# Performance work log

Hardware: AMD Instinct MI355X
Metric: run time of the kernel (lower is better)

Reference implementation:

```python
import jax, jax.numpy as jnp
import numpy as np


def bilinear_sample(img, xs, ys):
    # img: [C,H,W]; xs, ys: [Ho,Wo] fractional source coords (pixel units).
    # Zero-fill outside the image, matching grid_sample(padding_mode='zeros').
    C, H, W = img.shape
    x0f = jnp.floor(xs); y0f = jnp.floor(ys)
    wx = xs - x0f; wy = ys - y0f
    x0 = x0f.astype(jnp.int32); y0 = y0f.astype(jnp.int32)

    def gather(yi, xi):
        inb = ((xi >= 0) & (xi <= W - 1) & (yi >= 0) & (yi <= H - 1))
        xc = jnp.clip(xi, 0, W - 1); yc = jnp.clip(yi, 0, H - 1)
        return img[:, yc, xc] * inb[None].astype(img.dtype)

    v00 = gather(y0,     x0)
    v01 = gather(y0,     x0 + 1)
    v10 = gather(y0 + 1, x0)
    v11 = gather(y0 + 1, x0 + 1)
    return (v00 * (1 - wx) * (1 - wy) + v01 * wx * (1 - wy)
            + v10 * (1 - wx) * wy + v11 * wx * wy)


def setup_inputs() -> dict:
    key = jax.random.key(0)
    k1, k2 = jax.random.split(key)
    frame = jax.random.uniform(k1, (1, 4, 1080, 1920), dtype=jnp.float32)
    # last channel is the alpha/transparency mask: fully opaque frame
    frame = frame.at[:, -1].set(1.0)
    canvas = jax.random.uniform(k2, (1, 4, 2048, 3072), dtype=jnp.float32)
    # realistic near-identity homography: small rotation + translation + tiny perspective
    th = 0.02
    Hmat = jnp.array([[np.cos(th), -np.sin(th), 400.0],
                      [np.sin(th),  np.cos(th), 300.0],
                      [1e-6,        0.0,        1.0]], dtype=jnp.float32)
    return {"frame": frame, "Hmat": Hmat, "canvas": canvas}


def reference(frame, Hmat, canvas):
    # Homography warp of `frame` into the canvas coordinate grid (inverse warp +
    # bilinear resample), then 'over' alpha-compositing onto the canvas
    # (merge_frame), fused into one pass over the canvas buffer.
    _, C, Hc, Wc = canvas.shape
    Hinv = jnp.linalg.inv(Hmat)
    dt = frame.dtype
    ys, xs = jnp.meshgrid(jnp.arange(Hc, dtype=dt), jnp.arange(Wc, dtype=dt), indexing='ij')
    coords = jnp.stack([xs, ys, jnp.ones_like(xs)])          # [3,Hc,Wc]
    src = jnp.einsum('ij,jhw->ihw', Hinv, coords)            # [3,Hc,Wc]
    sx = src[0] / src[2]
    sy = src[1] / src[2]
    warped = bilinear_sample(frame[0], sx, sy)               # [C,Hc,Wc]
    a_s = warped[-1:]                                        # source alpha
    a_c = canvas[0, -1:]                                     # canvas alpha
    out_rgb = warped[:-1] * a_s + canvas[0, :-1] * a_c * (1.0 - a_s)
    out_a = a_s + a_c * (1.0 - a_s)
    return jnp.concatenate([out_rgb, out_a], axis=0)[None]   # [1,C,Hc,Wc]
```

## Files before the change

kernel.cpp:

```cpp
#include <hip/hip_runtime.h>


#define FH 1080
#define FW 1920
#define CH 2048
#define CW 3072
#define FHW (FH * FW)
#define CHW (CH * CW)

__global__ __launch_bounds__(256) void pano_kernel(
    const float* __restrict__ frame,
    const float* __restrict__ Hm,
    const float* __restrict__ canvas,
    float* __restrict__ out)
{
    const int x = blockIdx.x * 256 + threadIdx.x;
    const int y = blockIdx.y;
    const int pix = y * CW + x;

    const float a  = Hm[0], b  = Hm[1], c  = Hm[2];
    const float d  = Hm[3], e  = Hm[4], f  = Hm[5];
    const float g  = Hm[6], hh = Hm[7], i9 = Hm[8];

    const float A0 = e * i9 - f * hh, A1 = c * hh - b * i9, A2 = b * f - c * e;
    const float B0 = f * g  - d * i9, B1 = a * i9 - c * g,  B2 = c * d - a * f;
    const float C0 = d * hh - e * g,  C1 = b * g  - a * hh, C2 = a * e - b * d;

    const float xf = (float)x, yf = (float)y;
    const float u = A0 * xf + A1 * yf + A2;
    const float v = B0 * xf + B1 * yf + B2;
    const float w = C0 * xf + C1 * yf + C2;
    const float sx = u / w;
    const float sy = v / w;

    const float x0f = floorf(sx);
    const float y0f = floorf(sy);
    const float wx = sx - x0f;
    const float wy = sy - y0f;
    const int x0 = (int)x0f;
    const int y0 = (int)y0f;

    const float c0 = canvas[0 * CHW + pix];
    const float c1 = canvas[1 * CHW + pix];
    const float c2 = canvas[2 * CHW + pix];
    const float ac = canvas[3 * CHW + pix];

    float w0 = 0.f, w1 = 0.f, w2 = 0.f, as = 0.f;

    if (x0 >= -1 && x0 <= FW - 1 && y0 >= -1 && y0 <= FH - 1) {
        const int x1 = x0 + 1, y1 = y0 + 1;
        const float mx0 = (x0 >= 0 && x0 <= FW - 1) ? 1.f : 0.f;
        const float mx1 = (x1 >= 0 && x1 <= FW - 1) ? 1.f : 0.f;
        const float my0 = (y0 >= 0 && y0 <= FH - 1) ? 1.f : 0.f;
        const float my1 = (y1 >= 0 && y1 <= FH - 1) ? 1.f : 0.f;
        const int xc0 = min(max(x0, 0), FW - 1);
        const int xc1 = min(max(x1, 0), FW - 1);
        const int yc0 = min(max(y0, 0), FH - 1);
        const int yc1 = min(max(y1, 0), FH - 1);

        const float w00 = (1.f - wx) * (1.f - wy) * mx0 * my0;
        const float w01 = wx * (1.f - wy) * mx1 * my0;
        const float w10 = (1.f - wx) * wy * mx0 * my1;
        const float w11 = wx * wy * mx1 * my1;

        const int i00 = yc0 * FW + xc0;
        const int i01 = yc0 * FW + xc1;
        const int i10 = yc1 * FW + xc0;
        const int i11 = yc1 * FW + xc1;

        #pragma unroll
        for (int ch = 0; ch < 4; ++ch) {
            const float* fp = frame + ch * FHW;
            const float val = w00 * fp[i00] + w01 * fp[i01]
                            + w10 * fp[i10] + w11 * fp[i11];
            if (ch == 0) w0 = val;
            else if (ch == 1) w1 = val;
            else if (ch == 2) w2 = val;
            else as = val;
        }
    }

    const float k = ac * (1.f - as);
    out[0 * CHW + pix] = w0 * as + c0 * k;
    out[1 * CHW + pix] = w1 * as + c1 * k;
    out[2 * CHW + pix] = w2 * as + c2 * k;
    out[3 * CHW + pix] = as + k;
}

extern "C" void kernel_launch(void* const* d_in, const int* in_sizes, int n_in,
                              void* d_out, int out_size, void* d_ws, size_t ws_size,
                              hipStream_t stream) {
    const float* frame  = (const float*)d_in[0];
    const float* Hm     = (const float*)d_in[1];
    const float* canvas = (const float*)d_in[2];
    float* out = (float*)d_out;

    dim3 block(256, 1, 1);
    dim3 grid(CW / 256, CH, 1);
    pano_kernel<<<grid, block, 0, stream>>>(frame, Hm, canvas, out);
}
```

Baseline: 203.7 us.

## Process four pixels per thread with vector canvas I/O and nontemporal stores

Each thread now handles four consecutive canvas pixels. It loads the canvas with 128-bit vector loads and writes the output with nontemporal vector stores. The homography numerators are advanced incrementally, the division is replaced by a fast reciprocal, and a fully-interior fast path skips the clamping and masking. This aims to cut memory instruction count and per-pixel ALU overhead in a bandwidth-bound kernel. In exchange, each thread issues a serial chain of gathers, and the approximate reciprocal may differ slightly from the exact division.

After: 213.6 us. 1.05x slower.

```diff
diff --git a/kernel.cpp b/kernel.cpp
--- a/kernel.cpp
+++ b/kernel.cpp
@@ -8,15 +8,17 @@
 #define FHW (FH * FW)
 #define CHW (CH * CW)
 
+typedef float f32x4 __attribute__((ext_vector_type(4)));
+
 __global__ __launch_bounds__(256) void pano_kernel(
     const float* __restrict__ frame,
     const float* __restrict__ Hm,
     const float* __restrict__ canvas,
     float* __restrict__ out)
 {
-    const int x = blockIdx.x * 256 + threadIdx.x;
-    const int y = blockIdx.y;
-    const int pix = y * CW + x;
+    const int x4  = blockIdx.x * 1024 + threadIdx.x * 4;
+    const int y   = blockIdx.y;
+    const int pix = y * CW + x4;
 
     const float a  = Hm[0], b  = Hm[1], c  = Hm[2];
     const float d  = Hm[3], e  = Hm[4], f  = Hm[5];
@@ -26,65 +28,95 @@
     const float B0 = f * g  - d * i9, B1 = a * i9 - c * g,  B2 = c * d - a * f;
     const float C0 = d * hh - e * g,  C1 = b * g  - a * hh, C2 = a * e - b * d;
 
-    const float xf = (float)x, yf = (float)y;
-    const float u = A0 * xf + A1 * yf + A2;
-    const float v = B0 * xf + B1 * yf + B2;
-    const float w = C0 * xf + C1 * yf + C2;
-    const float sx = u / w;
-    const float sy = v / w;
+    const f32x4 cv0 = *(const f32x4*)(canvas + 0 * CHW + pix);
+    const f32x4 cv1 = *(const f32x4*)(canvas + 1 * CHW + pix);
+    const f32x4 cv2 = *(const f32x4*)(canvas + 2 * CHW + pix);
+    const f32x4 cva = *(const f32x4*)(canvas + 3 * CHW + pix);
 
-    const float x0f = floorf(sx);
-    const float y0f = floorf(sy);
-    const float wx = sx - x0f;
-    const float wy = sy - y0f;
-    const int x0 = (int)x0f;
-    const int y0 = (int)y0f;
+    const float xf = (float)x4, yf = (float)y;
+    float u = A0 * xf + A1 * yf + A2;
+    float v = B0 * xf + B1 * yf + B2;
+    float w = C0 * xf + C1 * yf + C2;
 
-    const float c0 = canvas[0 * CHW + pix];
-    const float c1 = canvas[1 * CHW + pix];
-    const float c2 = canvas[2 * CHW + pix];
-    const float ac = canvas[3 * CHW + pix];
+    f32x4 o0, o1, o2, oa;
 
-    float w0 = 0.f, w1 = 0.f, w2 = 0.f, as = 0.f;
+    #pragma unroll
+    for (int j = 0; j < 4; ++j) {
+        const float rw = __builtin_amdgcn_rcpf(w);
+        const float sx = u * rw;
+        const float sy = v * rw;
 
-    if (x0 >= -1 && x0 <= FW - 1 && y0 >= -1 && y0 <= FH - 1) {
-        const int x1 = x0 + 1, y1 = y0 + 1;
-        const float mx0 = (x0 >= 0 && x0 <= FW - 1) ? 1.f : 0.f;
-        const float mx1 = (x1 >= 0 && x1 <= FW - 1) ? 1.f : 0.f;
-        const float my0 = (y0 >= 0 && y0 <= FH - 1) ? 1.f : 0.f;
-        const float my1 = (y1 >= 0 && y1 <= FH - 1) ? 1.f : 0.f;
-        const int xc0 = min(max(x0, 0), FW - 1);
-        const int xc1 = min(max(x1, 0), FW - 1);
-        const int yc0 = min(max(y0, 0), FH - 1);
-        const int yc1 = min(max(y1, 0), FH - 1);
+        const float x0f = floorf(sx);
+        const float y0f = floorf(sy);
+        const float wx = sx - x0f;
+        const float wy = sy - y0f;
+        const int x0 = (int)x0f;
+        const int y0 = (int)y0f;
 
-        const float w00 = (1.f - wx) * (1.f - wy) * mx0 * my0;
-        const float w01 = wx * (1.f - wy) * mx1 * my0;
-        const float w10 = (1.f - wx) * wy * mx0 * my1;
-        const float w11 = wx * wy * mx1 * my1;
+        float w0 = 0.f, w1 = 0.f, w2 = 0.f, as = 0.f;
 
-        const int i00 = yc0 * FW + xc0;
-        const int i01 = yc0 * FW + xc1;
-        const int i10 = yc1 * FW + xc0;
-        const int i11 = yc1 * FW + xc1;
+        if (x0 >= 0 && x0 <= FW - 2 && y0 >= 0 && y0 <= FH - 2) {
+            const float w00 = (1.f - wx) * (1.f - wy);
+            const float w01 = wx * (1.f - wy);
+            const float w10 = (1.f - wx) * wy;
+            const float w11 = wx * wy;
+            const int i00 = y0 * FW + x0;
+            #pragma unroll
+            for (int ch = 0; ch < 4; ++ch) {
+                const float* fp = frame + ch * FHW;
+                const float val = w00 * fp[i00]      + w01 * fp[i00 + 1]
+                                + w10 * fp[i00 + FW] + w11 * fp[i00 + FW + 1];
+                if      (ch == 0) w0 = val;
+                else if (ch == 1) w1 = val;
+                else if (ch == 2) w2 = val;
+                else              as = val;
+            }
+        } else if (x0 >= -1 && x0 <= FW - 1 && y0 >= -1 && y0 <= FH - 1) {
+            const int x1 = x0 + 1, y1 = y0 + 1;
+            const float mx0 = (x0 >= 0) ? 1.f : 0.f;
+            const float mx1 = (x1 <= FW - 1) ? 1.f : 0.f;
+            const float my0 = (y0 >= 0) ? 1.f : 0.f;
+            const float my1 = (y1 <= FH - 1) ? 1.f : 0.f;
+            const int xc0 = min(max(x0, 0), FW - 1);
+            const int xc1 = min(max(x1, 0), FW - 1);
+            const int yc0 = min(max(y0, 0), FH - 1);
+            const int yc1 = min(max(y1, 0), FH - 1);
 
-        #pragma unroll
-        for (int ch = 0; ch < 4; ++ch) {
-            const float* fp = frame + ch * FHW;
-            const float val = w00 * fp[i00] + w01 * fp[i01]
-                            + w10 * fp[i10] + w11 * fp[i11];
-            if (ch == 0) w0 = val;
-            else if (ch == 1) w1 = val;
-            else if (ch == 2) w2 = val;
-            else as = val;
+            const float w00 = (1.f - wx) * (1.f - wy) * mx0 * my0;
+            const float w01 = wx * (1.f - wy) * mx1 * my0;
+            const float w10 = (1.f - wx) * wy * mx0 * my1;
+            const float w11 = wx * wy * mx1 * my1;
+
+            const int i00 = yc0 * FW + xc0;
+            const int i01 = yc0 * FW + xc1;
+            const int i10 = yc1 * FW + xc0;
+            const int i11 = yc1 * FW + xc1;
+
+            #pragma unroll
+            for (int ch = 0; ch < 4; ++ch) {
+                const float* fp = frame + ch * FHW;
+                const float val = w00 * fp[i00] + w01 * fp[i01]
+                                + w10 * fp[i10] + w11 * fp[i11];
+                if      (ch == 0) w0 = val;
+                else if (ch == 1) w1 = val;
+                else if (ch == 2) w2 = val;
+                else              as = val;
+            }
         }
+
+        const float k = cva[j] * (1.f - as);
+        o0[j] = w0 * as + cv0[j] * k;
+        o1[j] = w1 * as + cv1[j] * k;
+        o2[j] = w2 * as + cv2[j] * k;
+        oa[j] = as + k;
+
+        u += A0; v += B0; w += C0;
     }
 
-    const float k = ac * (1.f - as);
-    out[0 * CHW + pix] = w0 * as + c0 * k;
-    out[1 * CHW + pix] = w1 * as + c1 * k;
-    out[2 * CHW + pix] = w2 * as + c2 * k;
-    out[3 * CHW + pix] = as + k;
+    __builtin_nontemporal_store(o0, (f32x4*)(out + 0 * CHW + pix));
+    __builtin_nontemporal_store(o1, (f32x4*)(out + 1 * CHW + pix));
+    __builtin_nontemporal_store(o2, (f32x4*)(out + 2 * CHW + pix));
+    __builtin_nontemporal_store(oa, (f32x4*)(out + 3 * CHW + pix));
 }
 
 extern "C" void kernel_launch(void* const* d_in, const int* in_sizes, int n_in,
@@ -96,6 +128,6 @@
     float* out = (float*)d_out;
 
     dim3 block(256, 1, 1);
-    dim3 grid(CW / 256, CH, 1);
+    dim3 grid(CW / 1024, CH, 1);
     pano_kernel<<<grid, block, 0, stream>>>(frame, Hm, canvas, out);
 }
```
